# Kernel optimization log

Hardware: AMD Instinct MI355X
Metric: run time of the kernel (lower is better)

The kernel has to match this reference:

```python
import jax, jax.numpy as jnp
import numpy as np

B, T, C = 2, 2048, 1024
H, D = 16, 64


def setup_inputs() -> dict:
    key = jax.random.key(0)
    ks = jax.random.split(key, 5)
    s = 1.0 / np.sqrt(C)  # keep projections well-scaled
    return {
        "x": jax.random.normal(ks[0], (B, T, C), dtype=jnp.float32),
        "wq": jax.random.normal(ks[1], (C, C), dtype=jnp.float32) * s,
        "wk": jax.random.normal(ks[2], (C, C), dtype=jnp.float32) * s,
        "wv": jax.random.normal(ks[3], (C, C), dtype=jnp.float32) * s,
        "wo": jax.random.normal(ks[4], (C, C), dtype=jnp.float32) * s,
    }


def reference(x, wq, wk, wv, wo):
    # nn.Linear(d,d,bias=False): y = x @ W.T ; weights stored [out,in]
    q = (x @ wq.T).reshape(B, T, H, D).transpose(0, 2, 1, 3)  # [B,H,T,D]
    k = (x @ wk.T).reshape(B, T, H, D).transpose(0, 2, 1, 3)
    v = (x @ wv.T).reshape(B, T, H, D).transpose(0, 2, 1, 3)
    scale = jnp.sqrt(jnp.float32(D))
    scores = jnp.einsum("bhtd,bhsd->bhts", q, k) / scale  # [B,H,T,T]
    # additive causal mask: -inf above the diagonal
    causal = jnp.tril(jnp.ones((T, T), dtype=bool))
    scores = jnp.where(causal[None, None], scores, jnp.float32(-1e9))
    weights = jax.nn.softmax(scores, axis=-1)
    out = jnp.einsum("bhts,bhsd->bhtd", weights, v)  # [B,H,T,D]
    out = out.transpose(0, 2, 1, 3).reshape(B, T, C)
    return out @ wo.T
```

## Files before the change

kernel.cpp:

```cpp
#include <hip/hip_runtime.h>
#include <stdint.h>

#define B_ 2
#define T_ 2048
#define C_ 1024
#define H_ 16
#define D_ 64
#define M_ (B_*T_)

typedef __attribute__((ext_vector_type(8))) short bf16x8;
typedef __attribute__((ext_vector_type(4))) short bf16x4;
typedef __attribute__((ext_vector_type(4))) __bf16 bf16v4;
typedef __attribute__((ext_vector_type(4))) float f32x4;
typedef unsigned short u16;

#define MFMA32(a, b, c) __builtin_amdgcn_mfma_f32_16x16x32_bf16((a), (b), (c), 0, 0, 0)

__device__ __forceinline__ u16 f2bf(float f) {
  union { float f; uint32_t u; } v; v.f = f;
  uint32_t u = v.u;
  return (u16)((u + 0x7fffu + ((u >> 16) & 1u)) >> 16);
}

__device__ __forceinline__ float exp2_fast(float x) { return __builtin_amdgcn_exp2f(x); }

typedef const __attribute__((address_space(1))) void* gas_t;
typedef __attribute__((address_space(3))) void* las_t;
__device__ __forceinline__ void gld_lds16(const void* g, void* l) {
  __builtin_amdgcn_global_load_lds((gas_t)g, (las_t)l, 16, 0, 0);
}

__global__ void cvt_all(const float* __restrict__ x,
                        const float* __restrict__ w0, const float* __restrict__ w1,
                        const float* __restrict__ w2, const float* __restrict__ w3,
                        u16* __restrict__ xb,
                        u16* __restrict__ d0, u16* __restrict__ d1,
                        u16* __restrict__ d2, u16* __restrict__ d3) {
  size_t i = ((size_t)blockIdx.x * 256 + threadIdx.x) * 4;
  const float* s; u16* d; size_t off;
  const size_t NX = (size_t)M_ * C_;
  const size_t NW = (size_t)C_ * C_;
  if (i < NX) { s = x; d = xb; off = i; }
  else {
    size_t j = i - NX;
    int w = (int)(j / NW); off = j - (size_t)w * NW;
    switch (w) {
      case 0: s = w0; d = d0; break;
      case 1: s = w1; d = d1; break;
      case 2: s = w2; d = d2; break;
      default: s = w3; d = d3; break;
    }
  }
  float4 v = *(const float4*)(s + off);
  ushort4 o;
  o.x = f2bf(v.x); o.y = f2bf(v.y); o.z = f2bf(v.z); o.w = f2bf(v.w);
  *(ushort4*)(d + off) = o;
}

__device__ __forceinline__ void gemm_core(const u16* __restrict__ A,
                                          const u16* __restrict__ W,
                                          int m0, int n0, int Kt,
                                          f32x4 acc[4][4])
{
  __shared__ u16 As[128*64];
  __shared__ u16 Bs[128*64];
  const int t = threadIdx.x;
  const int lane = t & 63;
  const int wave = t >> 6;
  const int q = lane >> 4;
  const int l15 = lane & 15;
  const int wm = (wave >> 1) * 64;
  const int wn = (wave & 1) * 64;

  #pragma unroll
  for (int i = 0; i < 4; ++i)
    #pragma unroll
    for (int j = 0; j < 4; ++j)
      acc[i][j] = (f32x4){0.f, 0.f, 0.f, 0.f};

  for (int k0 = 0; k0 < Kt; k0 += 64) {
    #pragma unroll
    for (int r = 0; r < 4; ++r) {
      int Lc = r * 256 + t;
      int row = Lc >> 3;
      int gcc = (Lc & 7) ^ (row & 7);
      gld_lds16(A + (size_t)(m0 + row) * Kt + k0 + gcc * 8, As + Lc * 8);
    }
    #pragma unroll
    for (int r = 0; r < 4; ++r) {
      int Lc = r * 256 + t;
      int row = Lc >> 3;
      int gcc = (Lc & 7) ^ (row & 7);
      gld_lds16(W + (size_t)(n0 + row) * Kt + k0 + gcc * 8, Bs + Lc * 8);
    }
    __syncthreads();

    #pragma unroll
    for (int kk = 0; kk < 2; ++kk) {
      bf16x8 af[4], bfr[4];
      #pragma unroll
      for (int i = 0; i < 4; ++i) {
        int m = wm + i * 16 + l15;
        int ch = (kk * 4 + q) ^ (m & 7);
        af[i] = *(const bf16x8*)(As + m * 64 + ch * 8);
      }
      #pragma unroll
      for (int j = 0; j < 4; ++j) {
        int n = wn + j * 16 + l15;
        int ch = (kk * 4 + q) ^ (n & 7);
        bfr[j] = *(const bf16x8*)(Bs + n * 64 + ch * 8);
      }
      #pragma unroll
      for (int i = 0; i < 4; ++i)
        #pragma unroll
        for (int j = 0; j < 4; ++j)
          acc[i][j] = MFMA32(af[i], bfr[j], acc[i][j]);
    }
    __syncthreads();
  }
}

#define QSCALE 0.1803368801111244f
__global__ __launch_bounds__(256, 3)
void gemm_qkv(const u16* __restrict__ X,
              const u16* __restrict__ Wq, const u16* __restrict__ Wk,
              const u16* __restrict__ Wv,
              u16* __restrict__ Q, u16* __restrict__ K, u16* __restrict__ Vt)
{
  const int bm = blockIdx.x;
  const int bn = blockIdx.y;
  const int seg = bn >> 3;
  const int nb = (bn & 7) * 128;

  const int t = threadIdx.x, lane = t & 63, wave = t >> 6;
  const int q = lane >> 4, l15 = lane & 15;
  const int wm = (wave >> 1) * 64, wn = (wave & 1) * 64;

  f32x4 acc[4][4];

  if (seg < 2) {
    const u16* W = (seg == 0) ? Wq : Wk;
    gemm_core(W, X, nb, bm * 128, C_, acc);
    u16* dst = (seg == 0) ? Q : K;
    const float scale = (seg == 0) ? QSCALE : 1.0f;
    #pragma unroll
    for (int i = 0; i < 4; ++i) {
      #pragma unroll
      for (int j = 0; j < 4; ++j) {
        const int o = nb + wm + i * 16 + q * 4;
        const int h = o >> 6, d = o & 63;
        const int mtok = bm * 128 + wn + j * 16 + l15;
        const int b = mtok >> 11, tt = mtok & (T_ - 1);
        ushort4 pk;
        pk.x = f2bf(acc[i][j][0] * scale); pk.y = f2bf(acc[i][j][1] * scale);
        pk.z = f2bf(acc[i][j][2] * scale); pk.w = f2bf(acc[i][j][3] * scale);
        *(ushort4*)(dst + (((size_t)(b * H_ + h)) * T_ + tt) * D_ + d) = pk;
      }
    }
  } else {
    gemm_core(X, Wv, bm * 128, nb, C_, acc);
    #pragma unroll
    for (int i = 0; i < 4; ++i) {
      #pragma unroll
      for (int j = 0; j < 4; ++j) {
        const int mbase = bm * 128 + wm + i * 16 + q * 4;
        const int b = mbase >> 11, tt = mbase & (T_ - 1);
        const int n = nb + wn + j * 16 + l15;
        const int h = n >> 6, d = n & 63;
        const int ttp = (tt & ~31) | ((tt & 12) << 1) | ((tt & 16) >> 2);
        size_t idx = (((size_t)(b * H_ + h)) * D_ + d) * T_ + ttp;
        ushort4 pk;
        pk.x = f2bf(acc[i][j][0]); pk.y = f2bf(acc[i][j][1]);
        pk.z = f2bf(acc[i][j][2]); pk.w = f2bf(acc[i][j][3]);
        *(ushort4*)(Vt + idx) = pk;
      }
    }
  }
}

__global__ __launch_bounds__(256, 1)
void attn(const u16* __restrict__ Q, const u16* __restrict__ K,
          const u16* __restrict__ Vt, u16* __restrict__ Att)
{
  __shared__ u16 Ks[2][128 * 64];
  __shared__ u16 Vs[2][64 * 128];
  const int t = threadIdx.x;
  const int lane = t & 63, wave = t >> 6;
  const int q = lane >> 4, l15 = lane & 15;
  const int bh = blockIdx.x;
  const int pr = blockIdx.y;
  const int tix0 = pr, tix1 = 15 - pr, tix2 = 16 + pr, tix3 = 31 - pr;
  const u16* Qp = Q + (size_t)bh * T_ * D_;
  const u16* Kp = K + (size_t)bh * T_ * D_;
  const u16* Vp = Vt + (size_t)bh * D_ * T_;

  int rowg[4]; int qb[4];
  qb[0] = tix0 * 64; qb[1] = tix1 * 64; qb[2] = tix2 * 64; qb[3] = tix3 * 64;
  bf16x8 aq0[4], aq1[4];
  #pragma unroll
  for (int i = 0; i < 4; ++i) {
    rowg[i] = qb[i] + 4 * l15 + wave;
    const u16* qr = Qp + (size_t)rowg[i] * 64;
    aq0[i] = *(const bf16x8*)(qr + q * 8);
    aq1[i] = *(const bf16x8*)(qr + 32 + q * 8);
  }

  f32x4 o[4][4];
  float ls[4];
  #pragma unroll
  for (int i = 0; i < 4; ++i) {
    ls[i] = 0.f;
    #pragma unroll
    for (int j = 0; j < 4; ++j) o[i][j] = (f32x4){0.f, 0.f, 0.f, 0.f};
  }

  const int qb3 = qb[3];

  auto stage = [&](int kb, int buf) {
    #pragma unroll
    for (int r = 0; r < 4; ++r) {
      int c = r * 256 + t, row = c >> 3, gcc = (c & 7) ^ (row & 7);
      gld_lds16(Kp + (size_t)(kb + row) * 64 + gcc * 8, &Ks[buf][c * 8]);
    }
    #pragma unroll
    for (int r = 0; r < 4; ++r) {
      int c = r * 256 + t, row = c >> 4, gcc = (c & 15) ^ (row & 15);
      gld_lds16(Vp + (size_t)row * T_ + kb + gcc * 8, &Vs[buf][c * 8]);
    }
  };

  stage(0, 0);
  int cur = 0;
  for (int kb = 0; kb <= qb3; kb += 128, cur ^= 1) {
    __syncthreads();
    if (kb + 128 <= qb3) stage(kb + 128, cur ^ 1);
    const u16* Kc = &Ks[cur][0];
    const u16* Vc = &Vs[cur][0];

    #pragma unroll
    for (int s = 0; s < 2; ++s) {
      const int kbase = kb + s * 64;
      if (kbase > qb3) break;

      bf16x8 kf0[4], kf1[4];
      #pragma unroll
      for (int j2 = 0; j2 < 4; ++j2) {
        const int rw = s * 64 + j2 * 16 + l15;
        kf0[j2] = *(const bf16x8*)(Kc + rw * 64 + ((q)     ^ (rw & 7)) * 8);
        kf1[j2] = *(const bf16x8*)(Kc + rw * 64 + ((4 + q) ^ (rw & 7)) * 8);
      }
      bf16x8 vfrag[4][2];
      #pragma unroll
      for (int j = 0; j < 4; ++j) {
        const int rw = j * 16 + l15;
        #pragma unroll
        for (int kk = 0; kk < 2; ++kk) {
          const int cc = ((2 * s + kk) * 4 + q) ^ (rw & 15);
          vfrag[j][kk] = *(const bf16x8*)(Vc + rw * 128 + cc * 8);
        }
      }

      #pragma unroll
      for (int i = 0; i < 4; ++i) {
        if (kbase > qb[i]) continue;
        const bool diag = (kbase == qb[i]);
        bf16x4 pb[4];
        #pragma unroll
        for (int j2 = 0; j2 < 4; ++j2) {
          f32x4 z = (f32x4){0.f, 0.f, 0.f, 0.f};
          z = MFMA32(kf0[j2], aq0[i], z);
          z = MFMA32(kf1[j2], aq1[i], z);
          if (diag) {
            #pragma unroll
            for (int r = 0; r < 4; ++r) {
              const int key = kbase + j2 * 16 + q * 4 + r;
              if (key > rowg[i]) z[r] = -1e30f;
            }
          }
          float p0 = exp2_fast(z[0]), p1 = exp2_fast(z[1]);
          float p2 = exp2_fast(z[2]), p3 = exp2_fast(z[3]);
          ls[i] += (p0 + p1) + (p2 + p3);
          bf16v4 bv;
          bv[0] = (__bf16)p0; bv[1] = (__bf16)p1;
          bv[2] = (__bf16)p2; bv[3] = (__bf16)p3;
          pb[j2] = __builtin_bit_cast(bf16x4, bv);
        }
        #pragma unroll
        for (int kk = 0; kk < 2; ++kk) {
          const bf16x8 pc = __builtin_shufflevector(pb[2 * kk], pb[2 * kk + 1],
                                                    0, 1, 2, 3, 4, 5, 6, 7);
          #pragma unroll
          for (int j = 0; j < 4; ++j)
            o[i][j] = MFMA32(vfrag[j][kk], pc, o[i][j]);
        }
      }
    }
  }

  const int b = bh >> 4, h = bh & 15;
  #pragma unroll
  for (int i = 0; i < 4; ++i) {
    float l = ls[i];
    l += __shfl_xor(l, 16, 64); l += __shfl_xor(l, 32, 64);
    const float inv = __builtin_amdgcn_rcpf(l);
    #pragma unroll
    for (int j = 0; j < 4; ++j) {
      ushort4 pk;
      pk.x = f2bf(o[i][j][0] * inv); pk.y = f2bf(o[i][j][1] * inv);
      pk.z = f2bf(o[i][j][2] * inv); pk.w = f2bf(o[i][j][3] * inv);
      *(ushort4*)(Att + ((size_t)b * T_ + rowg[i]) * C_ + h * 64 + j * 16 + q * 4) = pk;
    }
  }
}

__global__ __launch_bounds__(256, 2)
void gemm_out(const u16* __restrict__ Att, const u16* __restrict__ Wo,
              float* __restrict__ Out)
{
  __shared__ u16 As[64 * 64];
  __shared__ u16 Bs[128 * 64];
  const int t = threadIdx.x;
  const int lane = t & 63, wave = t >> 6;
  const int q = lane >> 4, l15 = lane & 15;
  const int wm = (wave >> 1) * 32, wn = (wave & 1) * 64;
  const int m0 = blockIdx.x * 64;
  const int n0 = blockIdx.y * 128;

  f32x4 acc[2][4];
  #pragma unroll
  for (int i = 0; i < 2; ++i)
    #pragma unroll
    for (int j = 0; j < 4; ++j)
      acc[i][j] = (f32x4){0.f, 0.f, 0.f, 0.f};

  for (int k0 = 0; k0 < C_; k0 += 64) {
    #pragma unroll
    for (int r = 0; r < 2; ++r) {
      int Lc = r * 256 + t, row = Lc >> 3, gcc = (Lc & 7) ^ (row & 7);
      gld_lds16(Wo + (size_t)(m0 + row) * C_ + k0 + gcc * 8, As + Lc * 8);
    }
    #pragma unroll
    for (int r = 0; r < 4; ++r) {
      int Lc = r * 256 + t, row = Lc >> 3, gcc = (Lc & 7) ^ (row & 7);
      gld_lds16(Att + (size_t)(n0 + row) * C_ + k0 + gcc * 8, Bs + Lc * 8);
    }
    __syncthreads();

    #pragma unroll
    for (int kk = 0; kk < 2; ++kk) {
      bf16x8 af[2], bfr[4];
      #pragma unroll
      for (int i = 0; i < 2; ++i) {
        int m = wm + i * 16 + l15;
        int ch = (kk * 4 + q) ^ (m & 7);
        af[i] = *(const bf16x8*)(As + m * 64 + ch * 8);
      }
      #pragma unroll
      for (int j = 0; j < 4; ++j) {
        int n = wn + j * 16 + l15;
        int ch = (kk * 4 + q) ^ (n & 7);
        bfr[j] = *(const bf16x8*)(Bs + n * 64 + ch * 8);
      }
      #pragma unroll
      for (int i = 0; i < 2; ++i)
        #pragma unroll
        for (int j = 0; j < 4; ++j)
          acc[i][j] = MFMA32(af[i], bfr[j], acc[i][j]);
    }
    __syncthreads();
  }

  #pragma unroll
  for (int i = 0; i < 2; ++i) {
    #pragma unroll
    for (int j = 0; j < 4; ++j) {
      const int o = m0 + wm + i * 16 + q * 4;
      const int tok = n0 + wn + j * 16 + l15;
      float4 st = {acc[i][j][0], acc[i][j][1], acc[i][j][2], acc[i][j][3]};
      *(float4*)(Out + (size_t)tok * C_ + o) = st;
    }
  }
}

extern "C" void kernel_launch(void* const* d_in, const int* in_sizes, int n_in,
                              void* d_out, int out_size, void* d_ws, size_t ws_size,
                              hipStream_t stream) {
  const float* x  = (const float*)d_in[0];
  const float* wq = (const float*)d_in[1];
  const float* wk = (const float*)d_in[2];
  const float* wv = (const float*)d_in[3];
  const float* wo = (const float*)d_in[4];
  float* out = (float*)d_out;

  u16* ws  = (u16*)d_ws;
  u16* xb  = ws;
  u16* wqb = xb  + (size_t)M_ * C_;
  u16* wkb = wqb + (size_t)C_ * C_;
  u16* wvb = wkb + (size_t)C_ * C_;
  u16* wob = wvb + (size_t)C_ * C_;
  u16* Qb  = wob + (size_t)C_ * C_;
  u16* Kb  = Qb  + (size_t)M_ * C_;
  u16* Vtb = Kb  + (size_t)M_ * C_;
  u16* Atb = Vtb + (size_t)M_ * C_;

  cvt_all<<<dim3((M_ * C_ + 4 * C_ * C_) / 1024), 256, 0, stream>>>(
      x, wq, wk, wv, wo, xb, wqb, wkb, wvb, wob);

  gemm_qkv<<<dim3(M_ / 128, 24), 256, 0, stream>>>(xb, wqb, wkb, wvb, Qb, Kb, Vtb);
  attn<<<dim3(B_ * H_, 8), 256, 0, stream>>>(Qb, Kb, Vtb, Atb);
  gemm_out<<<dim3(C_ / 64, M_ / 128), 256, 0, stream>>>(Atb, wob, out);
}
```

Measured before the change: 171.1 us.

## Split attention key blocks across two wave groups with LDS reduction

The attention kernel now launches 512 threads, and the two 4-wave groups each process one 64-key half of every staged 128-key tile instead of one group looping over both halves. Partial output accumulators and row sums from the second group are reduced through shared memory before normalization and store. s_setprio hints are also added around the MFMA sections. This aims to double the waves per block to improve latency hiding on the 256-block grid, at the cost of an extra reduction pass and higher register and LDS pressure per block.

```diff
diff --git a/kernel.cpp b/kernel.cpp
--- a/kernel.cpp
+++ b/kernel.cpp
@@ -178,28 +178,29 @@
   }
 }
 
-__global__ __launch_bounds__(256, 1)
+__global__ __launch_bounds__(512, 2)
 void attn(const u16* __restrict__ Q, const u16* __restrict__ K,
           const u16* __restrict__ Vt, u16* __restrict__ Att)
 {
-  __shared__ u16 Ks[2][128 * 64];
-  __shared__ u16 Vs[2][64 * 128];
+  __shared__ u16 SM[32768 + 2048];
   const int t = threadIdx.x;
   const int lane = t & 63, wave = t >> 6;
+  const int w4 = wave & 3, wg = wave >> 2;
   const int q = lane >> 4, l15 = lane & 15;
   const int bh = blockIdx.x;
   const int pr = blockIdx.y;
-  const int tix0 = pr, tix1 = 15 - pr, tix2 = 16 + pr, tix3 = 31 - pr;
+  const int qb0 = pr * 64, qb1 = (15 - pr) * 64;
+  const int qb2 = (16 + pr) * 64, qb3 = (31 - pr) * 64;
+  int qb[4] = {qb0, qb1, qb2, qb3};
   const u16* Qp = Q + (size_t)bh * T_ * D_;
   const u16* Kp = K + (size_t)bh * T_ * D_;
   const u16* Vp = Vt + (size_t)bh * D_ * T_;
 
-  int rowg[4]; int qb[4];
-  qb[0] = tix0 * 64; qb[1] = tix1 * 64; qb[2] = tix2 * 64; qb[3] = tix3 * 64;
+  int rowg[4];
   bf16x8 aq0[4], aq1[4];
   #pragma unroll
   for (int i = 0; i < 4; ++i) {
-    rowg[i] = qb[i] + 4 * l15 + wave;
+    rowg[i] = qb[i] + 4 * l15 + w4;
     const u16* qr = Qp + (size_t)rowg[i] * 64;
     aq0[i] = *(const bf16x8*)(qr + q * 8);
     aq1[i] = *(const bf16x8*)(qr + 32 + q * 8);
@@ -214,18 +215,18 @@
     for (int j = 0; j < 4; ++j) o[i][j] = (f32x4){0.f, 0.f, 0.f, 0.f};
   }
 
-  const int qb3 = qb[3];
-
   auto stage = [&](int kb, int buf) {
-    #pragma unroll
-    for (int r = 0; r < 4; ++r) {
-      int c = r * 256 + t, row = c >> 3, gcc = (c & 7) ^ (row & 7);
-      gld_lds16(Kp + (size_t)(kb + row) * 64 + gcc * 8, &Ks[buf][c * 8]);
-    }
-    #pragma unroll
-    for (int r = 0; r < 4; ++r) {
-      int c = r * 256 + t, row = c >> 4, gcc = (c & 15) ^ (row & 15);
-      gld_lds16(Vp + (size_t)row * T_ + kb + gcc * 8, &Vs[buf][c * 8]);
+    u16* Ksb = SM + buf * 8192;
+    u16* Vsb = SM + 16384 + buf * 8192;
+    #pragma unroll
+    for (int r = 0; r < 2; ++r) {
+      int c = r * 512 + t, row = c >> 3, gcc = (c & 7) ^ (row & 7);
+      gld_lds16(Kp + (size_t)(kb + row) * 64 + gcc * 8, Ksb + c * 8);
+    }
+    #pragma unroll
+    for (int r = 0; r < 2; ++r) {
+      int c = r * 512 + t, row = c >> 4, gcc = (c & 15) ^ (row & 15);
+      gld_lds16(Vp + (size_t)row * T_ + kb + gcc * 8, Vsb + c * 8);
     }
   };
 
@@ -234,29 +235,26 @@
   for (int kb = 0; kb <= qb3; kb += 128, cur ^= 1) {
     __syncthreads();
     if (kb + 128 <= qb3) stage(kb + 128, cur ^ 1);
-    const u16* Kc = &Ks[cur][0];
-    const u16* Vc = &Vs[cur][0];
-
-    #pragma unroll
-    for (int s = 0; s < 2; ++s) {
-      const int kbase = kb + s * 64;
-      if (kbase > qb3) break;
-
+    const u16* Kc = SM + cur * 8192;
+    const u16* Vc = SM + 16384 + cur * 8192;
+
+    const int kbase = kb + wg * 64;
+    if (kbase <= qb3) {
       bf16x8 kf0[4], kf1[4];
       #pragma unroll
       for (int j2 = 0; j2 < 4; ++j2) {
-        const int rw = s * 64 + j2 * 16 + l15;
+        const int rw = wg * 64 + j2 * 16 + l15;
         kf0[j2] = *(const bf16x8*)(Kc + rw * 64 + ((q)     ^ (rw & 7)) * 8);
         kf1[j2] = *(const bf16x8*)(Kc + rw * 64 + ((4 + q) ^ (rw & 7)) * 8);
       }
-      bf16x8 vfrag[4][2];
+      bf16x8 vf[4][2];
       #pragma unroll
       for (int j = 0; j < 4; ++j) {
         const int rw = j * 16 + l15;
         #pragma unroll
         for (int kk = 0; kk < 2; ++kk) {
-          const int cc = ((2 * s + kk) * 4 + q) ^ (rw & 15);
-          vfrag[j][kk] = *(const bf16x8*)(Vc + rw * 128 + cc * 8);
+          const int cc = ((2 * wg + kk) * 4 + q) ^ (rw & 15);
+          vf[j][kk] = *(const bf16x8*)(Vc + rw * 128 + cc * 8);
         }
       }
 
@@ -268,8 +266,10 @@
         #pragma unroll
         for (int j2 = 0; j2 < 4; ++j2) {
           f32x4 z = (f32x4){0.f, 0.f, 0.f, 0.f};
+          __builtin_amdgcn_s_setprio(1);
           z = MFMA32(kf0[j2], aq0[i], z);
           z = MFMA32(kf1[j2], aq1[i], z);
+          __builtin_amdgcn_s_setprio(0);
           if (diag) {
             #pragma unroll
             for (int r = 0; r < 4; ++r) {
@@ -285,30 +285,57 @@
           bv[2] = (__bf16)p2; bv[3] = (__bf16)p3;
           pb[j2] = __builtin_bit_cast(bf16x4, bv);
         }
+        __builtin_amdgcn_s_setprio(1);
         #pragma unroll
         for (int kk = 0; kk < 2; ++kk) {
           const bf16x8 pc = __builtin_shufflevector(pb[2 * kk], pb[2 * kk + 1],
                                                     0, 1, 2, 3, 4, 5, 6, 7);
           #pragma unroll
           for (int j = 0; j < 4; ++j)
-            o[i][j] = MFMA32(vfrag[j][kk], pc, o[i][j]);
+            o[i][j] = MFMA32(vf[j][kk], pc, o[i][j]);
         }
-      }
-    }
-  }
-
-  const int b = bh >> 4, h = bh & 15;
-  #pragma unroll
-  for (int i = 0; i < 4; ++i) {
-    float l = ls[i];
-    l += __shfl_xor(l, 16, 64); l += __shfl_xor(l, 32, 64);
-    const float inv = __builtin_amdgcn_rcpf(l);
-    #pragma unroll
-    for (int j = 0; j < 4; ++j) {
-      ushort4 pk;
-      pk.x = f2bf(o[i][j][0] * inv); pk.y = f2bf(o[i][j][1] * inv);
-      pk.z = f2bf(o[i][j][2] * inv); pk.w = f2bf(o[i][j][3] * inv);
-      *(ushort4*)(Att + ((size_t)b * T_ + rowg[i]) * C_ + h * 64 + j * 16 + q * 4) = pk;
+        __builtin_amdgcn_s_setprio(0);
+      }
+    }
+  }
+
+  __syncthreads();
+  float4* red  = (float4*)SM;
+  float4* lred = (float4*)(SM + 32768);
+  if (wg == 1) {
+    #pragma unroll
+    for (int i = 0; i < 4; ++i)
+      #pragma unroll
+      for (int j = 0; j < 4; ++j) {
+        float4 v = {o[i][j][0], o[i][j][1], o[i][j][2], o[i][j][3]};
+        red[((i * 4 + w4) * 64 + lane) * 4 + j] = v;
+      }
+    float4 lv = {ls[0], ls[1], ls[2], ls[3]};
+    lred[w4 * 64 + lane] = lv;
+  }
+  __syncthreads();
+  if (wg == 0) {
+    const float4 lv = lred[w4 * 64 + lane];
+    ls[0] += lv.x; ls[1] += lv.y; ls[2] += lv.z; ls[3] += lv.w;
+    const int b = bh >> 4, h = bh & 15;
+    #pragma unroll
+    for (int i = 0; i < 4; ++i) {
+      #pragma unroll
+      for (int j = 0; j < 4; ++j) {
+        const float4 v = red[((i * 4 + w4) * 64 + lane) * 4 + j];
+        o[i][j][0] += v.x; o[i][j][1] += v.y;
+        o[i][j][2] += v.z; o[i][j][3] += v.w;
+      }
+      float l = ls[i];
+      l += __shfl_xor(l, 16, 64); l += __shfl_xor(l, 32, 64);
+      const float inv = __builtin_amdgcn_rcpf(l);
+      #pragma unroll
+      for (int j = 0; j < 4; ++j) {
+        ushort4 pk;
+        pk.x = f2bf(o[i][j][0] * inv); pk.y = f2bf(o[i][j][1] * inv);
+        pk.z = f2bf(o[i][j][2] * inv); pk.w = f2bf(o[i][j][3] * inv);
+        *(ushort4*)(Att + ((size_t)b * T_ + rowg[i]) * C_ + h * 64 + j * 16 + q * 4) = pk;
+      }
     }
   }
 }
@@ -407,6 +434,6 @@
       x, wq, wk, wv, wo, xb, wqb, wkb, wvb, wob);
 
   gemm_qkv<<<dim3(M_ / 128, 24), 256, 0, stream>>>(xb, wqb, wkb, wvb, Qb, Kb, Vtb);
-  attn<<<dim3(B_ * H_, 8), 256, 0, stream>>>(Qb, Kb, Vtb, Atb);
+  attn<<<dim3(B_ * H_, 8), 512, 0, stream>>>(Qb, Kb, Vtb, Atb);
   gemm_out<<<dim3(C_ / 64, M_ / 128), 256, 0, stream>>>(Atb, wob, out);
 }
```

Result: faster. 157.5 us, median of 2 (-8.0%).
